# Kernel tuning notes

Hardware: AMD Instinct MI355X
Metric: run time of the kernel (lower is better)

## Reference

```python
import jax, jax.numpy as jnp
import numpy as np

N = 100000
E = 1600000
F_IN = 128
HID = 64
N_CLASS = 40
NEG_SLOPE = 0.2


def setup_inputs() -> dict:
    key = jax.random.key(0)
    ks = jax.random.split(key, 16)
    s = lambda *sh: 1.0 / np.sqrt(sh[0])
    inp = {
        "x": jax.random.normal(ks[0], (N, F_IN), dtype=jnp.float32),
        "edge_index": jax.random.randint(ks[1], (2, E), 0, N, dtype=jnp.int64),
        "W1": jax.random.normal(ks[2], (F_IN, HID), jnp.float32) * s(F_IN),
        "b1": jnp.zeros((HID,), jnp.float32),
        "Wc0": jax.random.normal(ks[3], (HID, HID), jnp.float32) * s(HID),
        "att_src0": jax.random.normal(ks[4], (HID,), jnp.float32) * s(HID),
        "att_dst0": jax.random.normal(ks[5], (HID,), jnp.float32) * s(HID),
        "bias0": jnp.zeros((HID,), jnp.float32),
        "Wc1": jax.random.normal(ks[6], (HID, HID), jnp.float32) * s(HID),
        "att_src1": jax.random.normal(ks[7], (HID,), jnp.float32) * s(HID),
        "att_dst1": jax.random.normal(ks[8], (HID,), jnp.float32) * s(HID),
        "bias1": jnp.zeros((HID,), jnp.float32),
        "W2": jax.random.normal(ks[9], (HID, N_CLASS), jnp.float32) * s(HID),
        "b2": jnp.zeros((N_CLASS,), jnp.float32),
    }
    return inp


def gat_conv(x, src, dst, W, att_src, att_dst, bias):
    # x: [N, Fin]; src/dst: [E'] (self-loops already appended)
    h = x @ W                                   # [N, Fout]
    a_s = h @ att_src                           # [N]
    a_d = h @ att_dst                           # [N]
    e = jax.nn.leaky_relu(a_s[src] + a_d[dst], NEG_SLOPE)   # [E']
    # segment softmax over edges grouped by destination node
    e_max = jax.ops.segment_max(e, dst, num_segments=N)     # every node has a self-loop
    ex = jnp.exp(e - e_max[dst])
    denom = jax.ops.segment_sum(ex, dst, num_segments=N)
    alpha = ex / (denom[dst] + 1e-16)                        # [E']
    out = jax.ops.segment_sum(h[src] * alpha[:, None], dst, num_segments=N)
    return out + bias


def reference(x, edge_index, W1, b1, Wc0, att_src0, att_dst0, bias0,
              Wc1, att_src1, att_dst1, bias1, W2, b2):
    # eval mode: dropout_adj and feature dropout are identity
    loop = jnp.arange(N, dtype=edge_index.dtype)
    src = jnp.concatenate([edge_index[0], loop])
    dst = jnp.concatenate([edge_index[1], loop])

    h = jax.nn.relu(x @ W1 + b1)
    h = gat_conv(h, src, dst, Wc0, att_src0, att_dst0, bias0)
    h = jax.nn.relu(h)
    h = gat_conv(h, src, dst, Wc1, att_src1, att_dst1, bias1)
    logits = h @ W2 + b2
    return jax.nn.log_softmax(logits, axis=-1)
```

## Files before the change

### kernel.cpp

```cpp
#include <hip/hip_runtime.h>

#define N_NODES 100000
#define N_EDGES 1600000
#define F_IN    128
#define HID     64
#define N_CLASS 40
#define NEG_SLOPE 0.2f
#define ET (N_EDGES + N_NODES)
#define ROW_BLOCKS ((N_NODES + 63) / 64)

#define NCB   7
#define CAP1  294912
#define BPC   144
#define NFB   782
#define CAPF  2624
#define NT1   ((ET + 2047) / 2048)

typedef __attribute__((ext_vector_type(8))) short bf16x8;
typedef __attribute__((ext_vector_type(4))) float f32x4;

__device__ __forceinline__ unsigned int f2bf(float f) {
    unsigned int u = __float_as_uint(f);
    return (u + 0x7fffu + ((u >> 16) & 1u)) >> 16;
}

__global__ __launch_bounds__(256) void k_prepw(const float* __restrict__ W1,
        const float* __restrict__ Wc0, const float* __restrict__ Wc1,
        const float* __restrict__ W2,
        unsigned short* __restrict__ Wt1, unsigned short* __restrict__ Wtc0,
        unsigned short* __restrict__ Wtc1, unsigned short* __restrict__ W2t) {
    int t = threadIdx.x;
    for (int i = t; i < F_IN * HID; i += 256) {
        int k = i >> 6, n = i & 63;
        Wt1[n * F_IN + k] = (unsigned short)f2bf(W1[i]);
    }
    for (int i = t; i < HID * HID; i += 256) {
        int k = i >> 6, n = i & 63;
        Wtc0[n * HID + k] = (unsigned short)f2bf(Wc0[i]);
        Wtc1[n * HID + k] = (unsigned short)f2bf(Wc1[i]);
    }
    for (int i = t; i < 48 * HID; i += 256) {
        int n = i >> 6, k = i & 63;
        W2t[n * HID + k] = (n < N_CLASS)
            ? (unsigned short)f2bf(W2[k * N_CLASS + n]) : (unsigned short)0;
    }
}

__global__ __launch_bounds__(256) void k_lin1(const float* __restrict__ x,
        const unsigned short* __restrict__ Wt1, const float* __restrict__ b1,
        unsigned short* __restrict__ h0b) {
    __shared__ float xs[4][16 * 68];
    int t = threadIdx.x;
    int lane = t & 63, w = t >> 6;
    int quad = lane >> 4, lr = lane & 15;
    int rowg0 = blockIdx.x * 64 + w * 16;

    bf16x8 bfr[4][4];
    #pragma unroll
    for (int kc = 0; kc < 4; ++kc)
        #pragma unroll
        for (int nt = 0; nt < 4; ++nt)
            bfr[kc][nt] = *(const bf16x8*)(Wt1 + (nt * 16 + lr) * F_IN
                                           + kc * 32 + quad * 8);
    f32x4 zero = {0.f, 0.f, 0.f, 0.f};
    f32x4 acc[4] = {zero, zero, zero, zero};

    int arow = rowg0 + lr; if (arow >= N_NODES) arow = N_NODES - 1;
    const float* ab = x + (size_t)arow * F_IN;
    #pragma unroll
    for (int kc = 0; kc < 4; ++kc) {
        const float* ap = ab + kc * 32 + quad * 8;
        float4 a0 = *(const float4*)ap;
        float4 a1 = *(const float4*)(ap + 4);
        union { bf16x8 v; unsigned int u[4]; } af;
        af.u[0] = f2bf(a0.x) | (f2bf(a0.y) << 16);
        af.u[1] = f2bf(a0.z) | (f2bf(a0.w) << 16);
        af.u[2] = f2bf(a1.x) | (f2bf(a1.y) << 16);
        af.u[3] = f2bf(a1.z) | (f2bf(a1.w) << 16);
        #pragma unroll
        for (int nt = 0; nt < 4; ++nt)
            acc[nt] = __builtin_amdgcn_mfma_f32_16x16x32_bf16(
                          af.v, bfr[kc][nt], acc[nt], 0, 0, 0);
    }
    #pragma unroll
    for (int nt = 0; nt < 4; ++nt) {
        float bv = b1[nt * 16 + lr];
        #pragma unroll
        for (int reg = 0; reg < 4; ++reg)
            xs[w][(quad * 4 + reg) * 68 + nt * 16 + lr] =
                fmaxf(acc[nt][reg] + bv, 0.f);
    }
    __syncthreads();
    #pragma unroll
    for (int j = 0; j < 2; ++j) {
        int task = j * 64 + lane;
        int r = task >> 3, g = task & 7;
        int grow = blockIdx.x * 64 + w * 16 + r;
        if (grow < N_NODES) {
            const float* p = xs[w] + r * 68 + g * 8;
            uint4 u;
            u.x = f2bf(p[0]) | (f2bf(p[1]) << 16);
            u.y = f2bf(p[2]) | (f2bf(p[3]) << 16);
            u.z = f2bf(p[4]) | (f2bf(p[5]) << 16);
            u.w = f2bf(p[6]) | (f2bf(p[7]) << 16);
            *(uint4*)(h0b + (size_t)grow * HID + g * 8) = u;
        }
    }
}

__global__ __launch_bounds__(256) void k_gemm_att(
        const unsigned short* __restrict__ hin,
        const unsigned short* __restrict__ Wt,
        const float* __restrict__ att_s, const float* __restrict__ att_d,
        unsigned short* __restrict__ hb, float* __restrict__ as_,
        float* __restrict__ ad_) {
    __shared__ float xs[4][16 * 68];
    int t = threadIdx.x;
    int lane = t & 63, w = t >> 6;
    int quad = lane >> 4, lr = lane & 15;
    int rowg0 = blockIdx.x * 64 + w * 16;

    bf16x8 bfr[2][4];
    #pragma unroll
    for (int kc = 0; kc < 2; ++kc)
        #pragma unroll
        for (int nt = 0; nt < 4; ++nt)
            bfr[kc][nt] = *(const bf16x8*)(Wt + (nt * 16 + lr) * HID
                                           + kc * 32 + quad * 8);
    f32x4 zero = {0.f, 0.f, 0.f, 0.f};
    f32x4 acc[4] = {zero, zero, zero, zero};

    int arow = rowg0 + lr; if (arow >= N_NODES) arow = N_NODES - 1;
    #pragma unroll
    for (int kc = 0; kc < 2; ++kc) {
        bf16x8 af = *(const bf16x8*)(hin + (size_t)arow * HID
                                     + kc * 32 + quad * 8);
        #pragma unroll
        for (int nt = 0; nt < 4; ++nt)
            acc[nt] = __builtin_amdgcn_mfma_f32_16x16x32_bf16(
                          af, bfr[kc][nt], acc[nt], 0, 0, 0);
    }
    float asv[4], adv[4];
    #pragma unroll
    for (int nt = 0; nt < 4; ++nt) {
        asv[nt] = att_s[nt * 16 + lr];
        adv[nt] = att_d[nt * 16 + lr];
    }
    #pragma unroll
    for (int reg = 0; reg < 4; ++reg) {
        float p1 = acc[0][reg] * asv[0] + acc[1][reg] * asv[1]
                 + acc[2][reg] * asv[2] + acc[3][reg] * asv[3];
        float p2 = acc[0][reg] * adv[0] + acc[1][reg] * adv[1]
                 + acc[2][reg] * adv[2] + acc[3][reg] * adv[3];
        #pragma unroll
        for (int off = 1; off < 16; off <<= 1) {
            p1 += __shfl_xor(p1, off, 64);
            p2 += __shfl_xor(p2, off, 64);
        }
        if (lr == 0) {
            int grow = rowg0 + quad * 4 + reg;
            if (grow < N_NODES) { as_[grow] = p1; ad_[grow] = p2; }
        }
    }
    #pragma unroll
    for (int nt = 0; nt < 4; ++nt)
        #pragma unroll
        for (int reg = 0; reg < 4; ++reg)
            xs[w][(quad * 4 + reg) * 68 + nt * 16 + lr] = acc[nt][reg];
    __syncthreads();
    #pragma unroll
    for (int j = 0; j < 2; ++j) {
        int task = j * 64 + lane;
        int r = task >> 3, g = task & 7;
        int grow = blockIdx.x * 64 + w * 16 + r;
        if (grow < N_NODES) {
            const float* p = xs[w] + r * 68 + g * 8;
            uint4 u;
            u.x = f2bf(p[0]) | (f2bf(p[1]) << 16);
            u.y = f2bf(p[2]) | (f2bf(p[3]) << 16);
            u.z = f2bf(p[4]) | (f2bf(p[5]) << 16);
            u.w = f2bf(p[6]) | (f2bf(p[7]) << 16);
            *(uint4*)(hb + (size_t)grow * HID + g * 8) = u;
        }
    }
}

__global__ __launch_bounds__(256) void k_part1(const int* __restrict__ ei,
        int* __restrict__ tail1, int2* __restrict__ buf1) {
    __shared__ int2 eb[2048];
    __shared__ int hist[NCB], lbase[NCB], loff[NCB], goff[NCB];
    int t = threadIdx.x;
    int tileBase = blockIdx.x * 2048;
    int total = ET - tileBase; if (total > 2048) total = 2048;
    if (t < NCB) hist[t] = 0;
    __syncthreads();

    int sr[8], dr[8];
    #pragma unroll
    for (int r = 0; r < 8; ++r) {
        int i = tileBase + r * 256 + t;
        int s = -1, d = -1;
        if (i < ET) {
            if (i < N_EDGES) { s = ei[i]; d = ei[N_EDGES + i]; }
            else             { s = d = i - N_EDGES; }
            atomicAdd(&hist[d >> 14], 1);
        }
        sr[r] = s; dr[r] = d;
    }
    __syncthreads();
    if (t == 0) {
        int run = 0;
        for (int b = 0; b < NCB; ++b) { lbase[b] = run; loff[b] = 0; run += hist[b]; }
    }
    __syncthreads();
    if (t < NCB && hist[t] > 0) goff[t] = atomicAdd(&tail1[t], hist[t]);
    #pragma unroll
    for (int r = 0; r < 8; ++r) {
        if (dr[r] >= 0) {
            int b = dr[r] >> 14;
            int p = lbase[b] + atomicAdd(&loff[b], 1);
            eb[p] = make_int2(sr[r], dr[r]);
        }
    }
    __syncthreads();
    for (int j = t; j < total; j += 256) {
        int2 e = eb[j];
        int b = e.y >> 14;
        buf1[(size_t)b * CAP1 + goff[b] + (j - lbase[b])] = e;
    }
}

__global__ __launch_bounds__(256) void k_part2(const int2* __restrict__ buf1,
        const int* __restrict__ tail1, int* __restrict__ fcnt,
        int2* __restrict__ buf2) {
    __shared__ int2 eb[2048];
    __shared__ int hist[128], lbase[128], loff[128], goff[128], sc[128];
    int t = threadIdx.x;
    int cb   = blockIdx.x / BPC;
    int tile = blockIdx.x % BPC;
    int n1 = tail1[cb];
    int base = tile * 2048;
    if (base >= n1) return;
    int total = n1 - base; if (total > 2048) total = 2048;
    if (t < 128) hist[t] = 0;
    __syncthreads();

    int sr[8], dr[8];
    #pragma unroll
    for (int r = 0; r < 8; ++r) {
        int i = base + r * 256 + t;
        int s = -1, d = -1;
        if (i < n1) {
            int2 e = buf1[(size_t)cb * CAP1 + i];
            s = e.x; d = e.y;
            atomicAdd(&hist[(d >> 7) & 127], 1);
        }
        sr[r] = s; dr[r] = d;
    }
    __syncthreads();
    if (t < 128) sc[t] = hist[t];
    __syncthreads();
    for (int off = 1; off < 128; off <<= 1) {
        int u = (t < 128 && t >= off) ? sc[t - off] : 0;
        __syncthreads();
        if (t < 128) sc[t] += u;
        __syncthreads();
    }
    if (t < 128) { lbase[t] = sc[t] - hist[t]; loff[t] = 0; }
    __syncthreads();
    if (t < 128 && hist[t] > 0)
        goff[t] = atomicAdd(&fcnt[cb * 128 + t], hist[t]);
    #pragma unroll
    for (int r = 0; r < 8; ++r) {
        if (dr[r] >= 0) {
            int f = (dr[r] >> 7) & 127;
            int p = lbase[f] + atomicAdd(&loff[f], 1);
            eb[p] = make_int2(sr[r], dr[r]);
        }
    }
    __syncthreads();
    for (int j = t; j < total; j += 256) {
        int2 e = eb[j];
        int f = (e.y >> 7) & 127;
        buf2[(size_t)(e.y >> 7) * CAPF + goff[f] + (j - lbase[f])] = e;
    }
}

__global__ __launch_bounds__(1024) void k_fscan(const int* __restrict__ fcnt,
        int* __restrict__ fbase, int* __restrict__ rowptr) {
    __shared__ int s[1024];
    int t = threadIdx.x;
    int v = (t < NFB) ? fcnt[t] : 0;
    s[t] = v;
    __syncthreads();
    for (int off = 1; off < 1024; off <<= 1) {
        int u = (t >= off) ? s[t - off] : 0;
        __syncthreads();
        s[t] += u;
        __syncthreads();
    }
    if (t < NFB) fbase[t] = s[t] - v;
    if (t == 0) rowptr[N_NODES] = ET;
}

__global__ __launch_bounds__(256) void k_part3(const int2* __restrict__ buf2,
        const int* __restrict__ fcnt, const int* __restrict__ fbase,
        int* __restrict__ rowptr, int* __restrict__ col) {
    __shared__ int2 eb[CAPF];
    __shared__ int cs[CAPF];
    __shared__ int hist[128], lbase[128], loff[128], sc[128];
    int t = threadIdx.x;
    int fb = blockIdx.x;
    int nF = fcnt[fb];
    int gb = fbase[fb];
    int dbase = fb * 128;
    if (t < 128) hist[t] = 0;
    __syncthreads();
    for (int j = t; j < nF; j += 256) {
        int2 e = buf2[(size_t)fb * CAPF + j];
        eb[j] = e;
        atomicAdd(&hist[e.y - dbase], 1);
    }
    __syncthreads();
    if (t < 128) sc[t] = hist[t];
    __syncthreads();
    for (int off = 1; off < 128; off <<= 1) {
        int u = (t < 128 && t >= off) ? sc[t - off] : 0;
        __syncthreads();
        if (t < 128) sc[t] += u;
        __syncthreads();
    }
    if (t < 128) { lbase[t] = sc[t] - hist[t]; loff[t] = 0; }
    __syncthreads();
    if (t < 128 && dbase + t < N_NODES) rowptr[dbase + t] = gb + lbase[t];
    for (int j = t; j < nF; j += 256) {
        int2 e = eb[j];
        int r = e.y - dbase;
        int p = lbase[r] + atomicAdd(&loff[r], 1);
        cs[p] = e.x;
    }
    __syncthreads();
    for (int j = t; j < nF; j += 256) col[gb + j] = cs[j];
}

__global__ __launch_bounds__(256) void k_dhist(const int* __restrict__ rowptr,
        int* __restrict__ dhist) {
    __shared__ int lh[64];
    int t = threadIdx.x;
    if (t < 64) lh[t] = 0;
    __syncthreads();
    int i = blockIdx.x * 256 + t;
    if (i < N_NODES) {
        int deg = rowptr[i + 1] - rowptr[i];
        if (deg > 63) deg = 63;
        atomicAdd(&lh[deg], 1);
    }
    __syncthreads();
    if (t < 64 && lh[t] > 0) atomicAdd(&dhist[t], lh[t]);
}

__global__ __launch_bounds__(64) void k_dscan(const int* __restrict__ dhist,
        int* __restrict__ dbase) {
    int t = threadIdx.x;
    int v = dhist[t];
    int s = v;
    #pragma unroll
    for (int off = 1; off < 64; off <<= 1) {
        int u = __shfl_up(s, off, 64);
        if (t >= off) s += u;
    }
    dbase[t] = s - v;
}

__global__ __launch_bounds__(256) void k_dscatter(const int* __restrict__ rowptr,
        int* __restrict__ dbase, int* __restrict__ nodeord) {
    __shared__ int lh[64], goff[64];
    int t = threadIdx.x;
    if (t < 64) lh[t] = 0;
    __syncthreads();
    int i = blockIdx.x * 256 + t;
    int deg = -1, lrank = 0;
    if (i < N_NODES) {
        deg = rowptr[i + 1] - rowptr[i];
        if (deg > 63) deg = 63;
        lrank = atomicAdd(&lh[deg], 1);
    }
    __syncthreads();
    if (t < 64) goff[t] = (lh[t] > 0) ? atomicAdd(&dbase[t], lh[t]) : 0;
    __syncthreads();
    if (deg >= 0) nodeord[goff[deg] + lrank] = i;
}

template <bool RELU>
__global__ __launch_bounds__(256) void k_gat_agg(const int* __restrict__ rowptr,
        const int* __restrict__ col, const unsigned short* __restrict__ hb,
        const float* __restrict__ as_, const float* __restrict__ ad_,
        const float* __restrict__ bias, const int* __restrict__ nodeord,
        unsigned short* __restrict__ outb) {
    int t = threadIdx.x;
    int lane = t & 63;
    int wid = blockIdx.x * 4 + (t >> 6);
    int l8 = lane & 7;
    int ch = l8 * 8;
    int d = nodeord[wid * 8 + (lane >> 3)];
    int beg = rowptr[d];
    int deg = rowptr[d + 1] - beg;
    float add = ad_[d];
    int degw = deg;
    degw = max(degw, __shfl_xor(degw, 8, 64));
    degw = max(degw, __shfl_xor(degw, 16, 64));
    degw = max(degw, __shfl_xor(degw, 32, 64));

    float a0=0.f,a1=0.f,a2=0.f,a3=0.f,a4=0.f,a5=0.f,a6=0.f,a7=0.f,den=0.f;
    const unsigned short* hch = hb + ch;
    for (int c = 0; c < degw; c += 8) {
        int idx = c + l8;
        int sj = 0; float wj = 0.f;
        if (idx < deg) {
            sj = col[beg + idx];
            float e = as_[sj] + add;
            e = (e > 0.f) ? e : NEG_SLOPE * e;
            wj = __expf(e);
        }
        #pragma unroll
        for (int j = 0; j < 8; ++j) {
            int sl = (lane & 56) | j;
            int   s  = __shfl(sj, sl, 64);
            float w0 = __shfl(wj, sl, 64);
            den += w0;
            uint4 hv = *(const uint4*)(hch + (size_t)s * HID);
            a0 = fmaf(w0, __uint_as_float(hv.x << 16),         a0);
            a1 = fmaf(w0, __uint_as_float(hv.x & 0xffff0000u), a1);
            a2 = fmaf(w0, __uint_as_float(hv.y << 16),         a2);
            a3 = fmaf(w0, __uint_as_float(hv.y & 0xffff0000u), a3);
            a4 = fmaf(w0, __uint_as_float(hv.z << 16),         a4);
            a5 = fmaf(w0, __uint_as_float(hv.z & 0xffff0000u), a5);
            a6 = fmaf(w0, __uint_as_float(hv.w << 16),         a6);
            a7 = fmaf(w0, __uint_as_float(hv.w & 0xffff0000u), a7);
        }
    }
    float inv = 1.f / (den + 1e-16f);
    float4 bA = *(const float4*)(bias + ch);
    float4 bB = *(const float4*)(bias + ch + 4);
    float o0 = fmaf(a0, inv, bA.x), o1 = fmaf(a1, inv, bA.y);
    float o2 = fmaf(a2, inv, bA.z), o3 = fmaf(a3, inv, bA.w);
    float o4 = fmaf(a4, inv, bB.x), o5 = fmaf(a5, inv, bB.y);
    float o6 = fmaf(a6, inv, bB.z), o7 = fmaf(a7, inv, bB.w);
    if (RELU) {
        o0 = fmaxf(o0, 0.f); o1 = fmaxf(o1, 0.f);
        o2 = fmaxf(o2, 0.f); o3 = fmaxf(o3, 0.f);
        o4 = fmaxf(o4, 0.f); o5 = fmaxf(o5, 0.f);
        o6 = fmaxf(o6, 0.f); o7 = fmaxf(o7, 0.f);
    }
    uint4 u;
    u.x = f2bf(o0) | (f2bf(o1) << 16);
    u.y = f2bf(o2) | (f2bf(o3) << 16);
    u.z = f2bf(o4) | (f2bf(o5) << 16);
    u.w = f2bf(o6) | (f2bf(o7) << 16);
    *(uint4*)(outb + (size_t)d * HID + ch) = u;
}

__global__ __launch_bounds__(256) void k_final(
        const unsigned short* __restrict__ aggb,
        const unsigned short* __restrict__ W2t, const float* __restrict__ b2,
        float* __restrict__ out) {
    __shared__ float xs[64 * 44];
    int t = threadIdx.x;
    int lane = t & 63, w = t >> 6;
    int quad = lane >> 4, lr = lane & 15;
    int rowg0 = blockIdx.x * 64 + w * 16;
    int base = blockIdx.x * 64;
    int rem = N_NODES - base; if (rem > 64) rem = 64;

    bf16x8 bfr[2][3];
    #pragma unroll
    for (int kc = 0; kc < 2; ++kc)
        #pragma unroll
        for (int nt = 0; nt < 3; ++nt)
            bfr[kc][nt] = *(const bf16x8*)(W2t + (nt * 16 + lr) * HID
                                           + kc * 32 + quad * 8);
    f32x4 zero = {0.f, 0.f, 0.f, 0.f};
    f32x4 acc[3] = {zero, zero, zero};
    int arow = rowg0 + lr; if (arow >= N_NODES) arow = N_NODES - 1;
    #pragma unroll
    for (int kc = 0; kc < 2; ++kc) {
        bf16x8 af = *(const bf16x8*)(aggb + (size_t)arow * HID
                                     + kc * 32 + quad * 8);
        #pragma unroll
        for (int nt = 0; nt < 3; ++nt)
            acc[nt] = __builtin_amdgcn_mfma_f32_16x16x32_bf16(
                          af, bfr[kc][nt], acc[nt], 0, 0, 0);
    }
    float bc[3];
    #pragma unroll
    for (int nt = 0; nt < 3; ++nt) {
        int cl = nt * 16 + lr;
        bc[nt] = (cl < N_CLASS) ? b2[cl] : -1e30f;
    }
    #pragma unroll
    for (int reg = 0; reg < 4; ++reg) {
        float v0 = acc[0][reg] + bc[0];
        float v1 = acc[1][reg] + bc[1];
        float v2 = acc[2][reg] + bc[2];
        float m = fmaxf(fmaxf(v0, v1), v2);
        #pragma unroll
        for (int off = 1; off < 16; off <<= 1)
            m = fmaxf(m, __shfl_xor(m, off, 64));
        float ss = __expf(v0 - m) + __expf(v1 - m) + __expf(v2 - m);
        #pragma unroll
        for (int off = 1; off < 16; off <<= 1)
            ss += __shfl_xor(ss, off, 64);
        float lse = m + logf(ss);
        int r = w * 16 + quad * 4 + reg;
        xs[r * 44 + lr]      = v0 - lse;
        xs[r * 44 + 16 + lr] = v1 - lse;
        if (lr < 8) xs[r * 44 + 32 + lr] = v2 - lse;
    }
    __syncthreads();
    #pragma unroll
    for (int j = 0; j < 3; ++j) {
        int idx = j * 256 + t;
        if (idx < rem * 10) {
            int r = idx / 10, c4 = idx - r * 10;
            float4 v = *(const float4*)(xs + r * 44 + c4 * 4);
            *(float4*)(out + (size_t)base * N_CLASS + idx * 4) = v;
        }
    }
}

extern "C" void kernel_launch(void* const* d_in, const int* in_sizes, int n_in,
                              void* d_out, int out_size, void* d_ws, size_t ws_size,
                              hipStream_t stream) {
    const float* x     = (const float*)d_in[0];
    const int*   ei    = (const int*)  d_in[1];
    const float* W1    = (const float*)d_in[2];
    const float* b1    = (const float*)d_in[3];
    const float* Wc0   = (const float*)d_in[4];
    const float* as0   = (const float*)d_in[5];
    const float* ad0   = (const float*)d_in[6];
    const float* bias0 = (const float*)d_in[7];
    const float* Wc1   = (const float*)d_in[8];
    const float* as1   = (const float*)d_in[9];
    const float* ad1   = (const float*)d_in[10];
    const float* bias1 = (const float*)d_in[11];
    const float* W2    = (const float*)d_in[12];
    const float* b2    = (const float*)d_in[13];
    float* out = (float*)d_out;

    char* basep = (char*)d_ws;
    char* R1 = basep;
    char* R2 = basep + (size_t)N_NODES * HID * 4;
    unsigned short* h0b   = (unsigned short*)R1;
    unsigned short* agg1b = (unsigned short*)R1;
    int*            nodeord = (int*)(R1 + (size_t)N_NODES * HID * 2);
    int2*           buf2  = (int2*)R1;
    unsigned short* hb    = (unsigned short*)R2;
    unsigned short* agg0b = (unsigned short*)(R2 + (size_t)N_NODES * HID * 2);
    int2*           buf1  = (int2*)R2;

    char* mp = R2 + (size_t)N_NODES * HID * 4;
    unsigned short* Wt1  = (unsigned short*)mp;  mp += F_IN * HID * 2;
    unsigned short* Wtc0 = (unsigned short*)mp;  mp += HID * HID * 2;
    unsigned short* Wtc1 = (unsigned short*)mp;  mp += HID * HID * 2;
    unsigned short* W2t  = (unsigned short*)mp;  mp += 48 * HID * 2;
    float* as_   = (float*)mp;                   mp += N_NODES * 4;
    float* ad_   = (float*)mp;                   mp += N_NODES * 4;
    int*   col   = (int*)mp;                     mp += (size_t)ET * 4;
    int*   tail1 = (int*)mp;                     mp += NCB * 4;
    int*   fcnt  = (int*)mp;                     mp += NFB * 4;
    int*   fbase = (int*)mp;                     mp += NFB * 4;
    int*   dhist = (int*)mp;                     mp += 64 * 4;
    int*   dbase = (int*)mp;                     mp += 64 * 4;
    int*   rowptr= (int*)mp;

    const int AGG_BLOCKS = N_NODES / 32;
    const int NODE_BLOCKS = (N_NODES + 255) / 256;

    hipMemsetAsync(tail1, 0, (NCB + 2 * NFB + 128) * sizeof(int), stream);
    k_prepw<<<1, 256, 0, stream>>>(W1, Wc0, Wc1, W2, Wt1, Wtc0, Wtc1, W2t);
    k_part1<<<NT1, 256, 0, stream>>>(ei, tail1, buf1);
    k_part2<<<NCB * BPC, 256, 0, stream>>>(buf1, tail1, fcnt, buf2);
    k_fscan<<<1, 1024, 0, stream>>>(fcnt, fbase, rowptr);
    k_part3<<<NFB, 256, 0, stream>>>(buf2, fcnt, fbase, rowptr, col);
    k_dhist<<<NODE_BLOCKS, 256, 0, stream>>>(rowptr, dhist);
    k_dscan<<<1, 64, 0, stream>>>(dhist, dbase);
    k_dscatter<<<NODE_BLOCKS, 256, 0, stream>>>(rowptr, dbase, nodeord);

    k_lin1<<<ROW_BLOCKS, 256, 0, stream>>>(x, Wt1, b1, h0b);

    k_gemm_att<<<ROW_BLOCKS, 256, 0, stream>>>(h0b, Wtc0, as0, ad0,
                                               hb, as_, ad_);
    k_gat_agg<true><<<AGG_BLOCKS, 256, 0, stream>>>(
        rowptr, col, hb, as_, ad_, bias0, nodeord, agg0b);

    k_gemm_att<<<ROW_BLOCKS, 256, 0, stream>>>(agg0b, Wtc1, as1, ad1,
                                               hb, as_, ad_);
    k_gat_agg<false><<<AGG_BLOCKS, 256, 0, stream>>>(
        rowptr, col, hb, as_, ad_, bias1, nodeord, agg1b);

    k_final<<<ROW_BLOCKS, 256, 0, stream>>>(agg1b, W2t, b2, out);
}
```

Baseline: 319.4 us.

## Fuse lin1 with first GAT projection and fold degree histogram into partition

Merges the input linear layer with the first conv's GEMM and attention-score computation, keeping the ReLU output in LDS instead of writing and rereading h0b. The degree histogram is computed inside k_part3 from per-node counts, removing k_dhist. The workspace memset is folded into the weight-prep kernel, removing a separate memset launch. Weight fragments are now loaded per k-chunk rather than all upfront, reducing register pressure at the cost of interleaved loads.

After: 313.0 us. 2.0% less time.

```diff
diff --git a/kernel.cpp b/kernel.cpp
--- a/kernel.cpp
+++ b/kernel.cpp
@@ -28,8 +28,10 @@
         const float* __restrict__ Wc0, const float* __restrict__ Wc1,
         const float* __restrict__ W2,
         unsigned short* __restrict__ Wt1, unsigned short* __restrict__ Wtc0,
-        unsigned short* __restrict__ Wtc1, unsigned short* __restrict__ W2t) {
-    int t = threadIdx.x;
+        unsigned short* __restrict__ Wtc1, unsigned short* __restrict__ W2t,
+        int* __restrict__ zbuf, int zcount) {
+    int t = threadIdx.x;
+    for (int i = t; i < zcount; i += 256) zbuf[i] = 0;
     for (int i = t; i < F_IN * HID; i += 256) {
         int k = i >> 6, n = i & 63;
         Wt1[n * F_IN + k] = (unsigned short)f2bf(W1[i]);
@@ -46,29 +48,29 @@
     }
 }
 
-__global__ __launch_bounds__(256) void k_lin1(const float* __restrict__ x,
+__global__ __launch_bounds__(256) void k_lin1att(const float* __restrict__ x,
         const unsigned short* __restrict__ Wt1, const float* __restrict__ b1,
-        unsigned short* __restrict__ h0b) {
+        const unsigned short* __restrict__ Wtc0,
+        const float* __restrict__ att_s, const float* __restrict__ att_d,
+        unsigned short* __restrict__ hb, float* __restrict__ as_,
+        float* __restrict__ ad_) {
     __shared__ float xs[4][16 * 68];
     int t = threadIdx.x;
     int lane = t & 63, w = t >> 6;
     int quad = lane >> 4, lr = lane & 15;
     int rowg0 = blockIdx.x * 64 + w * 16;
 
-    bf16x8 bfr[4][4];
-    #pragma unroll
-    for (int kc = 0; kc < 4; ++kc)
-        #pragma unroll
-        for (int nt = 0; nt < 4; ++nt)
-            bfr[kc][nt] = *(const bf16x8*)(Wt1 + (nt * 16 + lr) * F_IN
-                                           + kc * 32 + quad * 8);
     f32x4 zero = {0.f, 0.f, 0.f, 0.f};
     f32x4 acc[4] = {zero, zero, zero, zero};
-
     int arow = rowg0 + lr; if (arow >= N_NODES) arow = N_NODES - 1;
     const float* ab = x + (size_t)arow * F_IN;
     #pragma unroll
     for (int kc = 0; kc < 4; ++kc) {
+        bf16x8 bw[4];
+        #pragma unroll
+        for (int nt = 0; nt < 4; ++nt)
+            bw[nt] = *(const bf16x8*)(Wt1 + (nt * 16 + lr) * F_IN
+                                      + kc * 32 + quad * 8);
         const float* ap = ab + kc * 32 + quad * 8;
         float4 a0 = *(const float4*)ap;
         float4 a1 = *(const float4*)(ap + 4);
@@ -80,7 +82,7 @@
         #pragma unroll
         for (int nt = 0; nt < 4; ++nt)
             acc[nt] = __builtin_amdgcn_mfma_f32_16x16x32_bf16(
-                          af.v, bfr[kc][nt], acc[nt], 0, 0, 0);
+                          af.v, bw[nt], acc[nt], 0, 0, 0);
     }
     #pragma unroll
     for (int nt = 0; nt < 4; ++nt) {
@@ -90,89 +92,59 @@
             xs[w][(quad * 4 + reg) * 68 + nt * 16 + lr] =
                 fmaxf(acc[nt][reg] + bv, 0.f);
     }
-    __syncthreads();
+    f32x4 acc2[4] = {zero, zero, zero, zero};
+    #pragma unroll
+    for (int kc = 0; kc < 2; ++kc) {
+        bf16x8 bw[4];
+        #pragma unroll
+        for (int nt = 0; nt < 4; ++nt)
+            bw[nt] = *(const bf16x8*)(Wtc0 + (nt * 16 + lr) * HID
+                                      + kc * 32 + quad * 8);
+        const float* ap = xs[w] + lr * 68 + kc * 32 + quad * 8;
+        float4 a0 = *(const float4*)ap;
+        float4 a1 = *(const float4*)(ap + 4);
+        union { bf16x8 v; unsigned int u[4]; } af;
+        af.u[0] = f2bf(a0.x) | (f2bf(a0.y) << 16);
+        af.u[1] = f2bf(a0.z) | (f2bf(a0.w) << 16);
+        af.u[2] = f2bf(a1.x) | (f2bf(a1.y) << 16);
+        af.u[3] = f2bf(a1.z) | (f2bf(a1.w) << 16);
+        #pragma unroll
+        for (int nt = 0; nt < 4; ++nt)
+            acc2[nt] = __builtin_amdgcn_mfma_f32_16x16x32_bf16(
+                          af.v, bw[nt], acc2[nt], 0, 0, 0);
+    }
+    float asv[4], adv[4];
+    #pragma unroll
+    for (int nt = 0; nt < 4; ++nt) {
+        asv[nt] = att_s[nt * 16 + lr];
+        adv[nt] = att_d[nt * 16 + lr];
+    }
+    #pragma unroll
+    for (int reg = 0; reg < 4; ++reg) {
+        float p1 = acc2[0][reg] * asv[0] + acc2[1][reg] * asv[1]
+                 + acc2[2][reg] * asv[2] + acc2[3][reg] * asv[3];
+        float p2 = acc2[0][reg] * adv[0] + acc2[1][reg] * adv[1]
+                 + acc2[2][reg] * adv[2] + acc2[3][reg] * adv[3];
+        #pragma unroll
+        for (int off = 1; off < 16; off <<= 1) {
+            p1 += __shfl_xor(p1, off, 64);
+            p2 += __shfl_xor(p2, off, 64);
+        }
+        if (lr == 0) {
+            int grow = rowg0 + quad * 4 + reg;
+            if (grow < N_NODES) { as_[grow] = p1; ad_[grow] = p2; }
+        }
+    }
+    #pragma unroll
+    for (int nt = 0; nt < 4; ++nt)
+        #pragma unroll
+        for (int reg = 0; reg < 4; ++reg)
+            xs[w][(quad * 4 + reg) * 68 + nt * 16 + lr] = acc2[nt][reg];
     #pragma unroll
     for (int j = 0; j < 2; ++j) {
         int task = j * 64 + lane;
         int r = task >> 3, g = task & 7;
-        int grow = blockIdx.x * 64 + w * 16 + r;
-        if (grow < N_NODES) {
-            const float* p = xs[w] + r * 68 + g * 8;
-            uint4 u;
-            u.x = f2bf(p[0]) | (f2bf(p[1]) << 16);
-            u.y = f2bf(p[2]) | (f2bf(p[3]) << 16);
-            u.z = f2bf(p[4]) | (f2bf(p[5]) << 16);
-            u.w = f2bf(p[6]) | (f2bf(p[7]) << 16);
-            *(uint4*)(h0b + (size_t)grow * HID + g * 8) = u;
-        }
-    }
-}
-
-__global__ __launch_bounds__(256) void k_gemm_att(
-        const unsigned short* __restrict__ hin,
-        const unsigned short* __restrict__ Wt,
-        const float* __restrict__ att_s, const float* __restrict__ att_d,
-        unsigned short* __restrict__ hb, float* __restrict__ as_,
-        float* __restrict__ ad_) {
-    __shared__ float xs[4][16 * 68];
-    int t = threadIdx.x;
-    int lane = t & 63, w = t >> 6;
-    int quad = lane >> 4, lr = lane & 15;
-    int rowg0 = blockIdx.x * 64 + w * 16;
-
-    bf16x8 bfr[2][4];
-    #pragma unroll
-    for (int kc = 0; kc < 2; ++kc)
-        #pragma unroll
-        for (int nt = 0; nt < 4; ++nt)
-            bfr[kc][nt] = *(const bf16x8*)(Wt + (nt * 16 + lr) * HID
-                                           + kc * 32 + quad * 8);
-    f32x4 zero = {0.f, 0.f, 0.f, 0.f};
-    f32x4 acc[4] = {zero, zero, zero, zero};
-
-    int arow = rowg0 + lr; if (arow >= N_NODES) arow = N_NODES - 1;
-    #pragma unroll
-    for (int kc = 0; kc < 2; ++kc) {
-        bf16x8 af = *(const bf16x8*)(hin + (size_t)arow * HID
-                                     + kc * 32 + quad * 8);
-        #pragma unroll
-        for (int nt = 0; nt < 4; ++nt)
-            acc[nt] = __builtin_amdgcn_mfma_f32_16x16x32_bf16(
-                          af, bfr[kc][nt], acc[nt], 0, 0, 0);
-    }
-    float asv[4], adv[4];
-    #pragma unroll
-    for (int nt = 0; nt < 4; ++nt) {
-        asv[nt] = att_s[nt * 16 + lr];
-        adv[nt] = att_d[nt * 16 + lr];
-    }
-    #pragma unroll
-    for (int reg = 0; reg < 4; ++reg) {
-        float p1 = acc[0][reg] * asv[0] + acc[1][reg] * asv[1]
-                 + acc[2][reg] * asv[2] + acc[3][reg] * asv[3];
-        float p2 = acc[0][reg] * adv[0] + acc[1][reg] * adv[1]
-                 + acc[2][reg] * adv[2] + acc[3][reg] * adv[3];
-        #pragma unroll
-        for (int off = 1; off < 16; off <<= 1) {
-            p1 += __shfl_xor(p1, off, 64);
-            p2 += __shfl_xor(p2, off, 64);
-        }
-        if (lr == 0) {
-            int grow = rowg0 + quad * 4 + reg;
-            if (grow < N_NODES) { as_[grow] = p1; ad_[grow] = p2; }
-        }
-    }
-    #pragma unroll
-    for (int nt = 0; nt < 4; ++nt)
-        #pragma unroll
-        for (int reg = 0; reg < 4; ++reg)
-            xs[w][(quad * 4 + reg) * 68 + nt * 16 + lr] = acc[nt][reg];
-    __syncthreads();
-    #pragma unroll
-    for (int j = 0; j < 2; ++j) {
-        int task = j * 64 + lane;
-        int r = task >> 3, g = task & 7;
-        int grow = blockIdx.x * 64 + w * 16 + r;
+        int grow = rowg0 + r;
         if (grow < N_NODES) {
             const float* p = xs[w] + r * 68 + g * 8;
             uint4 u;
@@ -185,6 +157,82 @@
     }
 }
 
+__global__ __launch_bounds__(256) void k_gemm_att(
+        const unsigned short* __restrict__ hin,
+        const unsigned short* __restrict__ Wt,
+        const float* __restrict__ att_s, const float* __restrict__ att_d,
+        unsigned short* __restrict__ hb, float* __restrict__ as_,
+        float* __restrict__ ad_) {
+    __shared__ float xs[4][16 * 68];
+    int t = threadIdx.x;
+    int lane = t & 63, w = t >> 6;
+    int quad = lane >> 4, lr = lane & 15;
+    int rowg0 = blockIdx.x * 64 + w * 16;
+
+    bf16x8 bfr[2][4];
+    #pragma unroll
+    for (int kc = 0; kc < 2; ++kc)
+        #pragma unroll
+        for (int nt = 0; nt < 4; ++nt)
+            bfr[kc][nt] = *(const bf16x8*)(Wt + (nt * 16 + lr) * HID
+                                           + kc * 32 + quad * 8);
+    f32x4 zero = {0.f, 0.f, 0.f, 0.f};
+    f32x4 acc[4] = {zero, zero, zero, zero};
+
+    int arow = rowg0 + lr; if (arow >= N_NODES) arow = N_NODES - 1;
+    #pragma unroll
+    for (int kc = 0; kc < 2; ++kc) {
+        bf16x8 af = *(const bf16x8*)(hin + (size_t)arow * HID
+                                     + kc * 32 + quad * 8);
+        #pragma unroll
+        for (int nt = 0; nt < 4; ++nt)
+            acc[nt] = __builtin_amdgcn_mfma_f32_16x16x32_bf16(
+                          af, bfr[kc][nt], acc[nt], 0, 0, 0);
+    }
+    float asv[4], adv[4];
+    #pragma unroll
+    for (int nt = 0; nt < 4; ++nt) {
+        asv[nt] = att_s[nt * 16 + lr];
+        adv[nt] = att_d[nt * 16 + lr];
+    }
+    #pragma unroll
+    for (int reg = 0; reg < 4; ++reg) {
+        float p1 = acc[0][reg] * asv[0] + acc[1][reg] * asv[1]
+                 + acc[2][reg] * asv[2] + acc[3][reg] * asv[3];
+        float p2 = acc[0][reg] * adv[0] + acc[1][reg] * adv[1]
+                 + acc[2][reg] * adv[2] + acc[3][reg] * adv[3];
+        #pragma unroll
+        for (int off = 1; off < 16; off <<= 1) {
+            p1 += __shfl_xor(p1, off, 64);
+            p2 += __shfl_xor(p2, off, 64);
+        }
+        if (lr == 0) {
+            int grow = rowg0 + quad * 4 + reg;
+            if (grow < N_NODES) { as_[grow] = p1; ad_[grow] = p2; }
+        }
+    }
+    #pragma unroll
+    for (int nt = 0; nt < 4; ++nt)
+        #pragma unroll
+        for (int reg = 0; reg < 4; ++reg)
+            xs[w][(quad * 4 + reg) * 68 + nt * 16 + lr] = acc[nt][reg];
+    #pragma unroll
+    for (int j = 0; j < 2; ++j) {
+        int task = j * 64 + lane;
+        int r = task >> 3, g = task & 7;
+        int grow = rowg0 + r;
+        if (grow < N_NODES) {
+            const float* p = xs[w] + r * 68 + g * 8;
+            uint4 u;
+            u.x = f2bf(p[0]) | (f2bf(p[1]) << 16);
+            u.y = f2bf(p[2]) | (f2bf(p[3]) << 16);
+            u.z = f2bf(p[4]) | (f2bf(p[5]) << 16);
+            u.w = f2bf(p[6]) | (f2bf(p[7]) << 16);
+            *(uint4*)(hb + (size_t)grow * HID + g * 8) = u;
+        }
+    }
+}
+
 __global__ __launch_bounds__(256) void k_part1(const int* __restrict__ ei,
         int* __restrict__ tail1, int2* __restrict__ buf1) {
     __shared__ int2 eb[2048];
@@ -305,21 +353,23 @@
 
 __global__ __launch_bounds__(256) void k_part3(const int2* __restrict__ buf2,
         const int* __restrict__ fcnt, const int* __restrict__ fbase,
-        int* __restrict__ rowptr, int* __restrict__ col) {
+        int* __restrict__ rowptr, int* __restrict__ col,
+        int* __restrict__ dhistg) {
     __shared__ int2 eb[CAPF];
     __shared__ int cs[CAPF];
-    __shared__ int hist[128], lbase[128], loff[128], sc[128];
+    __shared__ int hist[128], lbase[128], loff[128], sc[128], dh[64];
     int t = threadIdx.x;
     int fb = blockIdx.x;
     int nF = fcnt[fb];
     int gb = fbase[fb];
-    int dbase = fb * 128;
+    int nbase = fb * 128;
     if (t < 128) hist[t] = 0;
+    if (t >= 128 && t < 192) dh[t - 128] = 0;
     __syncthreads();
     for (int j = t; j < nF; j += 256) {
         int2 e = buf2[(size_t)fb * CAPF + j];
         eb[j] = e;
-        atomicAdd(&hist[e.y - dbase], 1);
+        atomicAdd(&hist[e.y - nbase], 1);
     }
     __syncthreads();
     if (t < 128) sc[t] = hist[t];
@@ -332,31 +382,20 @@
     }
     if (t < 128) { lbase[t] = sc[t] - hist[t]; loff[t] = 0; }
     __syncthreads();
-    if (t < 128 && dbase + t < N_NODES) rowptr[dbase + t] = gb + lbase[t];
+    if (t < 128 && nbase + t < N_NODES) {
+        rowptr[nbase + t] = gb + lbase[t];
+        int dg = hist[t]; if (dg > 63) dg = 63;
+        atomicAdd(&dh[dg], 1);
+    }
     for (int j = t; j < nF; j += 256) {
         int2 e = eb[j];
-        int r = e.y - dbase;
+        int r = e.y - nbase;
         int p = lbase[r] + atomicAdd(&loff[r], 1);
         cs[p] = e.x;
     }
     __syncthreads();
     for (int j = t; j < nF; j += 256) col[gb + j] = cs[j];
-}
-
-__global__ __launch_bounds__(256) void k_dhist(const int* __restrict__ rowptr,
-        int* __restrict__ dhist) {
-    __shared__ int lh[64];
-    int t = threadIdx.x;
-    if (t < 64) lh[t] = 0;
-    __syncthreads();
-    int i = blockIdx.x * 256 + t;
-    if (i < N_NODES) {
-        int deg = rowptr[i + 1] - rowptr[i];
-        if (deg > 63) deg = 63;
-        atomicAdd(&lh[deg], 1);
-    }
-    __syncthreads();
-    if (t < 64 && lh[t] > 0) atomicAdd(&dhist[t], lh[t]);
+    if (t < 64 && dh[t] > 0) atomicAdd(&dhistg[t], dh[t]);
 }
 
 __global__ __launch_bounds__(64) void k_dscan(const int* __restrict__ dhist,
@@ -550,7 +589,6 @@
     char* basep = (char*)d_ws;
     char* R1 = basep;
     char* R2 = basep + (size_t)N_NODES * HID * 4;
-    unsigned short* h0b   = (unsigned short*)R1;
     unsigned short* agg1b = (unsigned short*)R1;
     int*            nodeord = (int*)(R1 + (size_t)N_NODES * HID * 2);
     int2*           buf2  = (int2*)R1;
@@ -572,24 +610,22 @@
     int*   dhist = (int*)mp;                     mp += 64 * 4;
     int*   dbase = (int*)mp;                     mp += 64 * 4;
     int*   rowptr= (int*)mp;
+    const int ZCOUNT = NCB + 2 * NFB + 128;
 
     const int AGG_BLOCKS = N_NODES / 32;
     const int NODE_BLOCKS = (N_NODES + 255) / 256;
 
-    hipMemsetAsync(tail1, 0, (NCB + 2 * NFB + 128) * sizeof(int), stream);
-    k_prepw<<<1, 256, 0, stream>>>(W1, Wc0, Wc1, W2, Wt1, Wtc0, Wtc1, W2t);
+    k_prepw<<<1, 256, 0, stream>>>(W1, Wc0, Wc1, W2, Wt1, Wtc0, Wtc1, W2t,
+                                   tail1, ZCOUNT);
     k_part1<<<NT1, 256, 0, stream>>>(ei, tail1, buf1);
     k_part2<<<NCB * BPC, 256, 0, stream>>>(buf1, tail1, fcnt, buf2);
     k_fscan<<<1, 1024, 0, stream>>>(fcnt, fbase, rowptr);
-    k_part3<<<NFB, 256, 0, stream>>>(buf2, fcnt, fbase, rowptr, col);
-    k_dhist<<<NODE_BLOCKS, 256, 0, stream>>>(rowptr, dhist);
+    k_part3<<<NFB, 256, 0, stream>>>(buf2, fcnt, fbase, rowptr, col, dhist);
     k_dscan<<<1, 64, 0, stream>>>(dhist, dbase);
     k_dscatter<<<NODE_BLOCKS, 256, 0, stream>>>(rowptr, dbase, nodeord);
 
-    k_lin1<<<ROW_BLOCKS, 256, 0, stream>>>(x, Wt1, b1, h0b);
-
-    k_gemm_att<<<ROW_BLOCKS, 256, 0, stream>>>(h0b, Wtc0, as0, ad0,
-                                               hb, as_, ad_);
+    k_lin1att<<<ROW_BLOCKS, 256, 0, stream>>>(x, Wt1, b1, Wtc0, as0, ad0,
+                                              hb, as_, ad_);
     k_gat_agg<true><<<AGG_BLOCKS, 256, 0, stream>>>(
         rowptr, col, hb, as_, ad_, bias0, nodeord, agg0b);
 
```
